# Kernel optimization log

Measured on AMD Instinct MI355X. Metric: run time of the kernel, lower is better.

## Reference

```python
import jax, jax.numpy as jnp
import numpy as np

NC = 80          # num classes
NBINS = 16       # DFL bins = reg_max_bbox_loss + 1
REG_MAX = 15     # BboxLoss reg_max (m.reg_max - 1)
GAMMA = 1.5      # focal gamma (h['fl_gamma'])
ALPHA = 0.25     # focal alpha
BOX_W, CLS_W, DFL_W = 7.5, 0.5, 1.5
LEVELS = [(80, 80), (40, 40), (20, 20)]  # 640x640 image, strides 8/16/32


def make_anchor_points():
    pts = []
    for h, w in LEVELS:
        ys, xs = np.meshgrid(np.arange(h) + 0.5, np.arange(w) + 0.5, indexing='ij')
        pts.append(np.stack([xs.ravel(), ys.ravel()], -1))
    return jnp.asarray(np.concatenate(pts, 0), jnp.float32)  # (8400, 2)


def setup_inputs() -> dict:
    B, A = 32, 8400
    key = jax.random.key(0)
    k = jax.random.split(key, 6)
    anchor_points = make_anchor_points()
    pred_dist = jax.random.normal(k[0], (B, A, 4 * NBINS), jnp.float32)
    pred_scores = jax.random.normal(k[1], (B, A, NC), jnp.float32)
    fg_mask = jax.random.uniform(k[2], (B, A)) < 0.05
    # valid xyxy targets around each anchor -> ltrb in (0.5, 6) < REG_MAX - 0.01
    off1 = jax.random.uniform(k[3], (B, A, 2), minval=0.5, maxval=6.0)
    off2 = jax.random.uniform(k[4], (B, A, 2), minval=0.5, maxval=6.0)
    target_bboxes = jnp.concatenate([anchor_points - off1, anchor_points + off2], -1)
    target_scores = jax.random.uniform(k[5], (B, A, NC)) * fg_mask[..., None].astype(jnp.float32)
    return dict(pred_dist=pred_dist, pred_scores=pred_scores,
                anchor_points=anchor_points, target_bboxes=target_bboxes,
                target_scores=target_scores, fg_mask=fg_mask)


def _ciou(b1, b2, eps=1e-7):
    # xyxy CIoU, matches ultralytics bbox_iou(xywh=False, CIoU=True)
    b1x1, b1y1, b1x2, b1y2 = b1[..., 0], b1[..., 1], b1[..., 2], b1[..., 3]
    b2x1, b2y1, b2x2, b2y2 = b2[..., 0], b2[..., 1], b2[..., 2], b2[..., 3]
    w1, h1 = b1x2 - b1x1, b1y2 - b1y1 + eps
    w2, h2 = b2x2 - b2x1, b2y2 - b2y1 + eps
    inter = (jnp.minimum(b1x2, b2x2) - jnp.maximum(b1x1, b2x1)).clip(0) * \
            (jnp.minimum(b1y2, b2y2) - jnp.maximum(b1y1, b2y1)).clip(0)
    union = w1 * h1 + w2 * h2 - inter + eps
    iou = inter / union
    cw = jnp.maximum(b1x2, b2x2) - jnp.minimum(b1x1, b2x1)
    ch = jnp.maximum(b1y2, b2y2) - jnp.minimum(b1y1, b2y1)
    c2 = cw * cw + ch * ch + eps
    rho2 = ((b2x1 + b2x2 - b1x1 - b1x2) ** 2 + (b2y1 + b2y2 - b1y1 - b1y2) ** 2) / 4.0
    v = (4.0 / (jnp.pi ** 2)) * (jnp.arctan(w2 / h2) - jnp.arctan(w1 / h1)) ** 2
    alpha = jax.lax.stop_gradient(v / (v - iou + (1.0 + eps)))  # torch.no_grad()
    return iou - (rho2 / c2 + v * alpha)


def _loss_core(pred_dist, pred_scores, anchor_points, target_bboxes, target_scores, fg_mask):
    B, A, _ = pred_scores.shape
    dt = pred_scores.dtype
    tss = jnp.maximum(target_scores.sum(), 1.0)  # target_scores_sum

    # ---- focal BCE (pos_weight=1) ----
    p = jax.nn.sigmoid(pred_scores)
    bce = target_scores * jax.nn.softplus(-pred_scores) + (1.0 - target_scores) * jax.nn.softplus(pred_scores)
    p_t = target_scores * p + (1.0 - target_scores) * (1.0 - p)
    alpha_f = target_scores * ALPHA + (1.0 - target_scores) * (1.0 - ALPHA)
    loss_cls = (bce * alpha_f * (1.0 - p_t) ** GAMMA).sum() / tss

    # ---- bbox decode (DFL expectation) ----
    proj = jnp.arange(NBINS, dtype=dt)
    logits = pred_dist.reshape(B, A, 4, NBINS)
    dist = jax.nn.softmax(logits, axis=-1) @ proj                     # (B,A,4) ltrb
    pred_bboxes = jnp.concatenate([anchor_points - dist[..., :2],
                                   anchor_points + dist[..., 2:]], -1)

    fg = fg_mask.astype(dt)
    bbox_weight = target_scores.sum(-1) * fg                          # masked weight (B,A)

    # ---- CIoU loss (mask replaces masked_select) ----
    iou = _ciou(pred_bboxes, target_bboxes)
    loss_iou = ((1.0 - iou) * bbox_weight).sum() / tss

    # ---- DFL loss: left/right weighted cross-entropy ----
    target_ltrb = jnp.clip(jnp.concatenate([anchor_points - target_bboxes[..., :2],
                                            target_bboxes[..., 2:] - anchor_points], -1),
                           0.0, REG_MAX - 0.01)                       # (B,A,4)
    tl = jnp.floor(target_ltrb).astype(jnp.int32)
    tr = tl + 1
    wl = tr.astype(dt) - target_ltrb
    wr = 1.0 - wl
    logp = jax.nn.log_softmax(logits, axis=-1)                        # (B,A,4,NBINS)
    ce_l = -jnp.take_along_axis(logp, tl[..., None], axis=-1)[..., 0]
    ce_r = -jnp.take_along_axis(logp, tr[..., None], axis=-1)[..., 0]
    loss_dfl = (((ce_l * wl + ce_r * wr).mean(-1)) * bbox_weight).sum() / tss

    return jnp.stack([BOX_W * loss_iou, CLS_W * loss_cls, DFL_W * loss_dfl])


def reference(pred_dist, pred_scores, anchor_points, target_bboxes, target_scores, fg_mask):
    loss = _loss_core(pred_dist, pred_scores, anchor_points, target_bboxes, target_scores, fg_mask)
    return loss  # weighted [box, cls, dfl]; total = loss.sum()
```

## Files before the change

kernel.cpp:

```cpp
#include <hip/hip_runtime.h>
#include <math.h>

#define NC      80
#define A_TOT   8400
#define B_TOT   32
#define BA      (B_TOT * A_TOT)
#define NGRP    (BA / 16)
#define BLOCK   256
#define MAXNB   4200

__device__ __forceinline__ float wave_sum(float v) {
    #pragma unroll
    for (int off = 32; off > 0; off >>= 1) v += __shfl_down(v, off, 64);
    return v;
}

__global__ __launch_bounds__(BLOCK) void loss_main(
    const float* __restrict__ pred_dist,
    const float* __restrict__ pred_scores,
    const float* __restrict__ anchor_points,
    const float* __restrict__ target_bboxes,
    const float* __restrict__ target_scores,
    const int* __restrict__ fgmask,
    float* __restrict__ partials,
    int nb)
{
    __shared__ float red[4][4];

    const int tid  = threadIdx.x;
    const int lane = tid & 63;
    const int wid  = tid >> 6;
    const int q    = lane & 3;
    const int alg  = lane >> 2;
    const int gw   = blockIdx.x * 4 + wid;
    const int nw   = nb * 4;

    const float4* ps4 = (const float4*)pred_scores;
    const float4* ts4 = (const float4*)target_scores;
    const float4* tb4 = (const float4*)target_bboxes;

    float cls_acc = 0.0f, iou_acc = 0.0f, dfl_acc = 0.0f, ts_acc = 0.0f;

    for (int grp = gw; grp < NGRP; grp += nw) {
        const long g0   = (long)grp * 16;
        const long base = (g0 + alg) * 20 + q;

        const int fgm = fgmask[g0 + alg];

        float4 tvl[5];
        #pragma unroll
        for (int j = 0; j < 5; ++j) tvl[j] = make_float4(0.f, 0.f, 0.f, 0.f);
        if (fgm) {
            #pragma unroll
            for (int j = 0; j < 5; ++j) tvl[j] = ts4[base + 4 * j];
        }

        float rs = 0.0f;
        #pragma unroll
        for (int j = 0; j < 5; ++j) {
            float4 pv = ps4[base + 4 * j];
            float px[4] = {pv.x, pv.y, pv.z, pv.w};
            float tx[4] = {tvl[j].x, tvl[j].y, tvl[j].z, tvl[j].w};
            #pragma unroll
            for (int c = 0; c < 4; ++c) {
                float x  = px[c];
                float tv = tx[c];
                float e   = __expf(-fabsf(x));
                float ope = 1.0f + e;
                float lp  = __logf(ope);
                float sp  = fmaxf(x, 0.0f) + lp;
                float bce = sp - tv * x;
                float pp  = __builtin_amdgcn_rcpf(ope);
                float p   = (x >= 0.0f) ? pp : (1.0f - pp);
                float u   = fmaf(p, 1.0f - 2.0f * tv, tv);
                u = fmaxf(u, 0.0f);
                float af  = 0.75f - 0.5f * tv;
                float su  = __builtin_amdgcn_sqrtf(u);
                cls_acc += bce * af * (u * su);
                rs += tv;
            }
        }
        rs += __shfl_xor(rs, 1);
        rs += __shfl_xor(rs, 2);
        if (q == 0) ts_acc += rs;

        unsigned long long m = __ballot(rs > 0.0f && q == 0);
        while (m) {
            int b = __ffsll((long long)m) - 1;
            m &= m - 1;
            float w = __shfl(rs, b);
            const long g = g0 + (b >> 2);
            const int  a = (int)(g % A_TOT);
            const float ax = anchor_points[2 * a];
            const float ay = anchor_points[2 * a + 1];
            const float4 tb = tb4[g];

            const int side = lane >> 4;
            const int k    = lane & 15;

            float x = pred_dist[g * 64 + lane];

            float tval = (side == 0) ? ax - tb.x :
                         (side == 1) ? ay - tb.y :
                         (side == 2) ? tb.z - ax : tb.w - ay;
            float tcl = fminf(fmaxf(tval, 0.0f), 14.99f);
            int   tl  = (int)tcl;
            float wl  = (float)(tl + 1) - tcl;
            float wr  = 1.0f - wl;

            float mx = x;
            mx = fmaxf(mx, __shfl_xor(mx, 1));
            mx = fmaxf(mx, __shfl_xor(mx, 2));
            mx = fmaxf(mx, __shfl_xor(mx, 4));
            mx = fmaxf(mx, __shfl_xor(mx, 8));

            float ex = __expf(x - mx);
            float se = ex;
            float nu = (float)k * ex;
            float ls = ((k == tl) ? wl : (k == tl + 1) ? wr : 0.0f) * x;
            #pragma unroll
            for (int off = 1; off < 16; off <<= 1) {
                se += __shfl_xor(se, off);
                nu += __shfl_xor(nu, off);
                ls += __shfl_xor(ls, off);
            }
            float dist = nu * __builtin_amdgcn_rcpf(se);
            float ce   = mx + __logf(se) - ls;

            float d0 = __shfl(dist, 0),  d1 = __shfl(dist, 16);
            float d2 = __shfl(dist, 32), d3 = __shfl(dist, 48);
            float c0 = __shfl(ce, 0),    c1 = __shfl(ce, 16);
            float c2 = __shfl(ce, 32),   c3 = __shfl(ce, 48);

            if (lane == 0) {
                dfl_acc += 0.25f * (c0 + c1 + c2 + c3) * w;

                const float eps = 1e-7f;
                float px1 = ax - d0, py1 = ay - d1;
                float px2 = ax + d2, py2 = ay + d3;
                float w1 = px2 - px1, h1 = py2 - py1 + eps;
                float w2 = tb.z - tb.x, h2 = tb.w - tb.y + eps;
                float iw = fmaxf(fminf(px2, tb.z) - fmaxf(px1, tb.x), 0.0f);
                float ih = fmaxf(fminf(py2, tb.w) - fmaxf(py1, tb.y), 0.0f);
                float inter = iw * ih;
                float uni = w1 * h1 + w2 * h2 - inter + eps;
                float iou = inter / uni;
                float cw = fmaxf(px2, tb.z) - fminf(px1, tb.x);
                float ch = fmaxf(py2, tb.w) - fminf(py1, tb.y);
                float c2d = cw * cw + ch * ch + eps;
                float dx = tb.x + tb.z - px1 - px2;
                float dy = tb.y + tb.w - py1 - py2;
                float rho2 = (dx * dx + dy * dy) * 0.25f;
                const float c4pi2 = 0.40528473456935109f;
                float dat = atanf(w2 / h2) - atanf(w1 / h1);
                float v = c4pi2 * dat * dat;
                float alpha = v / (v - iou + (1.0f + eps));
                float ciou = iou - (rho2 / c2d + v * alpha);
                iou_acc += (1.0f - ciou) * w;
            }
        }
    }

    float v0 = wave_sum(iou_acc);
    float v1 = wave_sum(cls_acc);
    float v2 = wave_sum(ts_acc);
    float v3 = wave_sum(dfl_acc);
    if (lane == 0) { red[0][wid] = v0; red[1][wid] = v1; red[2][wid] = v2; red[3][wid] = v3; }
    __syncthreads();
    if (tid == 0) {
        float r0 = 0, r1 = 0, r2 = 0, r3 = 0;
        #pragma unroll
        for (int i = 0; i < 4; ++i) { r0 += red[0][i]; r1 += red[1][i]; r2 += red[2][i]; r3 += red[3][i]; }
        partials[0 * nb + blockIdx.x] = r0;
        partials[1 * nb + blockIdx.x] = r1;
        partials[2 * nb + blockIdx.x] = r2;
        partials[3 * nb + blockIdx.x] = r3;
    }
}

__global__ __launch_bounds__(BLOCK) void loss_reduce(
    const float* __restrict__ partials, int nb, float* __restrict__ out)
{
    __shared__ float red[4][4];
    int tid = threadIdx.x;
    float s0 = 0, s1 = 0, s2 = 0, s3 = 0;
    for (int i = tid; i < nb; i += BLOCK) {
        s0 += partials[i];
        s1 += partials[nb + i];
        s2 += partials[2 * nb + i];
        s3 += partials[3 * nb + i];
    }
    s0 = wave_sum(s0); s1 = wave_sum(s1); s2 = wave_sum(s2); s3 = wave_sum(s3);
    int wid = tid >> 6;
    if ((tid & 63) == 0) { red[0][wid] = s0; red[1][wid] = s1; red[2][wid] = s2; red[3][wid] = s3; }
    __syncthreads();
    if (tid == 0) {
        float r0 = 0, r1 = 0, r2 = 0, r3 = 0;
        #pragma unroll
        for (int i = 0; i < 4; ++i) { r0 += red[0][i]; r1 += red[1][i]; r2 += red[2][i]; r3 += red[3][i]; }
        float tss = fmaxf(r2, 1.0f);
        out[0] = 7.5f * r0 / tss;
        out[1] = 0.5f * r1 / tss;
        out[2] = 1.5f * r3 / tss;
    }
}

extern "C" void kernel_launch(void* const* d_in, const int* in_sizes, int n_in,
                              void* d_out, int out_size, void* d_ws, size_t ws_size,
                              hipStream_t stream) {
    const float* pred_dist     = (const float*)d_in[0];
    const float* pred_scores   = (const float*)d_in[1];
    const float* anchor_points = (const float*)d_in[2];
    const float* target_bboxes = (const float*)d_in[3];
    const float* target_scores = (const float*)d_in[4];
    const int*   fgmask        = (const int*)d_in[5];

    int nb = (int)(ws_size / (4 * sizeof(float)));
    if (nb > MAXNB) nb = MAXNB;
    if (nb < 1) nb = 1;

    float* partials = (float*)d_ws;
    loss_main<<<nb, BLOCK, 0, stream>>>(
        pred_dist, pred_scores, anchor_points, target_bboxes, target_scores,
        fgmask, partials, nb);
    loss_reduce<<<1, BLOCK, 0, stream>>>(partials, nb, (float*)d_out);
}
```

Before: 220.6 us.

## Split blocks into dedicated foreground DFL/CIoU and dense classification roles

Blocks are partitioned so one third scan the foreground mask in 64-anchor chunks and compute DFL and CIoU terms, prefetching the next foreground anchor's data while computing the current one. The remaining blocks run only the dense focal-BCE pass over scores and accumulate the target-score sum. This is meant to keep the latency-bound serial foreground loop from stalling the bandwidth-bound dense stream. The fixed one-third split risks load imbalance between the two roles.

New measurement: 216.1 us. 2.1% less time.

```diff
diff --git a/kernel.cpp b/kernel.cpp
--- a/kernel.cpp
+++ b/kernel.cpp
@@ -6,8 +6,9 @@
 #define B_TOT   32
 #define BA      (B_TOT * A_TOT)
 #define NGRP    (BA / 16)
+#define NCHUNK  (BA / 64)
 #define BLOCK   256
-#define MAXNB   4200
+#define NB_TARGET 3150
 
 __device__ __forceinline__ float wave_sum(float v) {
     #pragma unroll
@@ -23,17 +24,13 @@
     const float* __restrict__ target_scores,
     const int* __restrict__ fgmask,
     float* __restrict__ partials,
-    int nb)
+    int nb, int fgb)
 {
     __shared__ float red[4][4];
 
     const int tid  = threadIdx.x;
     const int lane = tid & 63;
     const int wid  = tid >> 6;
-    const int q    = lane & 3;
-    const int alg  = lane >> 2;
-    const int gw   = blockIdx.x * 4 + wid;
-    const int nw   = nb * 4;
 
     const float4* ps4 = (const float4*)pred_scores;
     const float4* ts4 = (const float4*)target_scores;
@@ -41,122 +38,147 @@
 
     float cls_acc = 0.0f, iou_acc = 0.0f, dfl_acc = 0.0f, ts_acc = 0.0f;
 
-    for (int grp = gw; grp < NGRP; grp += nw) {
-        const long g0   = (long)grp * 16;
-        const long base = (g0 + alg) * 20 + q;
-
-        const int fgm = fgmask[g0 + alg];
-
-        float4 tvl[5];
-        #pragma unroll
-        for (int j = 0; j < 5; ++j) tvl[j] = make_float4(0.f, 0.f, 0.f, 0.f);
-        if (fgm) {
+    if ((int)blockIdx.x < fgb) {
+        const int fstride = fgb * 4;
+        for (int c = blockIdx.x * 4 + wid; c < NCHUNK; c += fstride) {
+            const long abase = (long)c * 64;
+            const int myfg = fgmask[abase + lane];
+            unsigned long long m = __ballot(myfg != 0);
+
+            long gc = -1; float xc = 0.0f;
+            float4 tbc = make_float4(0,0,0,0), tsc = make_float4(0,0,0,0);
+            if (m) {
+                int b = __ffsll((long long)m) - 1; m &= m - 1;
+                gc = abase + b;
+                xc  = pred_dist[gc * 64 + lane];
+                tbc = tb4[gc];
+                tsc = (lane < 20) ? ts4[gc * 20 + lane] : make_float4(0,0,0,0);
+            }
+            while (gc >= 0) {
+                long gn = -1; float xn = 0.0f;
+                float4 tbn = make_float4(0,0,0,0), tsn = make_float4(0,0,0,0);
+                if (m) {
+                    int b = __ffsll((long long)m) - 1; m &= m - 1;
+                    gn = abase + b;
+                    xn  = pred_dist[gn * 64 + lane];
+                    tbn = tb4[gn];
+                    tsn = (lane < 20) ? ts4[gn * 20 + lane] : make_float4(0,0,0,0);
+                }
+
+                float w = tsc.x + tsc.y + tsc.z + tsc.w;
+                #pragma unroll
+                for (int off = 1; off < 64; off <<= 1) w += __shfl_xor(w, off, 64);
+
+                const int a = (int)(gc % A_TOT);
+                const float ax = anchor_points[2 * a];
+                const float ay = anchor_points[2 * a + 1];
+                const int side = lane >> 4;
+                const int k    = lane & 15;
+                const float x  = xc;
+
+                float tval = (side == 0) ? ax - tbc.x :
+                             (side == 1) ? ay - tbc.y :
+                             (side == 2) ? tbc.z - ax : tbc.w - ay;
+                float tcl = fminf(fmaxf(tval, 0.0f), 14.99f);
+                int   tl  = (int)tcl;
+                float wl  = (float)(tl + 1) - tcl;
+                float wr  = 1.0f - wl;
+
+                float mx = x;
+                mx = fmaxf(mx, __shfl_xor(mx, 1));
+                mx = fmaxf(mx, __shfl_xor(mx, 2));
+                mx = fmaxf(mx, __shfl_xor(mx, 4));
+                mx = fmaxf(mx, __shfl_xor(mx, 8));
+
+                float ex = __expf(x - mx);
+                float se = ex;
+                float nu = (float)k * ex;
+                float ls = ((k == tl) ? wl : (k == tl + 1) ? wr : 0.0f) * x;
+                #pragma unroll
+                for (int off = 1; off < 16; off <<= 1) {
+                    se += __shfl_xor(se, off);
+                    nu += __shfl_xor(nu, off);
+                    ls += __shfl_xor(ls, off);
+                }
+                float dist = nu * __builtin_amdgcn_rcpf(se);
+                float ce   = mx + __logf(se) - ls;
+
+                float d0 = __shfl(dist, 0),  d1 = __shfl(dist, 16);
+                float d2 = __shfl(dist, 32), d3 = __shfl(dist, 48);
+                float c0 = __shfl(ce, 0),    c1 = __shfl(ce, 16);
+                float c2 = __shfl(ce, 32),   c3 = __shfl(ce, 48);
+
+                if (lane == 0) {
+                    dfl_acc += 0.25f * (c0 + c1 + c2 + c3) * w;
+
+                    const float eps = 1e-7f;
+                    float px1 = ax - d0, py1 = ay - d1;
+                    float px2 = ax + d2, py2 = ay + d3;
+                    float w1 = px2 - px1, h1 = py2 - py1 + eps;
+                    float w2 = tbc.z - tbc.x, h2 = tbc.w - tbc.y + eps;
+                    float iw = fmaxf(fminf(px2, tbc.z) - fmaxf(px1, tbc.x), 0.0f);
+                    float ih = fmaxf(fminf(py2, tbc.w) - fmaxf(py1, tbc.y), 0.0f);
+                    float inter = iw * ih;
+                    float uni = w1 * h1 + w2 * h2 - inter + eps;
+                    float iou = inter / uni;
+                    float cw = fmaxf(px2, tbc.z) - fminf(px1, tbc.x);
+                    float ch = fmaxf(py2, tbc.w) - fminf(py1, tbc.y);
+                    float c2d = cw * cw + ch * ch + eps;
+                    float dx = tbc.x + tbc.z - px1 - px2;
+                    float dy = tbc.y + tbc.w - py1 - py2;
+                    float rho2 = (dx * dx + dy * dy) * 0.25f;
+                    const float c4pi2 = 0.40528473456935109f;
+                    float dat = atanf(w2 / h2) - atanf(w1 / h1);
+                    float v = c4pi2 * dat * dat;
+                    float alpha = v / (v - iou + (1.0f + eps));
+                    float ciou = iou - (rho2 / c2d + v * alpha);
+                    iou_acc += (1.0f - ciou) * w;
+                }
+
+                gc = gn; xc = xn; tbc = tbn; tsc = tsn;
+            }
+        }
+    } else {
+        const int q   = lane & 3;
+        const int alg = lane >> 2;
+        const int dstride = (nb - fgb) * 4;
+        for (int grp = (blockIdx.x - fgb) * 4 + wid; grp < NGRP; grp += dstride) {
+            const long g0   = (long)grp * 16;
+            const long base = (g0 + alg) * 20 + q;
+
+            const int fgm = fgmask[g0 + alg];
+
+            float4 tvl[5];
             #pragma unroll
-            for (int j = 0; j < 5; ++j) tvl[j] = ts4[base + 4 * j];
-        }
-
-        float rs = 0.0f;
-        #pragma unroll
-        for (int j = 0; j < 5; ++j) {
-            float4 pv = ps4[base + 4 * j];
-            float px[4] = {pv.x, pv.y, pv.z, pv.w};
-            float tx[4] = {tvl[j].x, tvl[j].y, tvl[j].z, tvl[j].w};
+            for (int j = 0; j < 5; ++j) tvl[j] = make_float4(0.f, 0.f, 0.f, 0.f);
+            if (fgm) {
+                #pragma unroll
+                for (int j = 0; j < 5; ++j) tvl[j] = ts4[base + 4 * j];
+            }
+
             #pragma unroll
-            for (int c = 0; c < 4; ++c) {
-                float x  = px[c];
-                float tv = tx[c];
-                float e   = __expf(-fabsf(x));
-                float ope = 1.0f + e;
-                float lp  = __logf(ope);
-                float sp  = fmaxf(x, 0.0f) + lp;
-                float bce = sp - tv * x;
-                float pp  = __builtin_amdgcn_rcpf(ope);
-                float p   = (x >= 0.0f) ? pp : (1.0f - pp);
-                float u   = fmaf(p, 1.0f - 2.0f * tv, tv);
-                u = fmaxf(u, 0.0f);
-                float af  = 0.75f - 0.5f * tv;
-                float su  = __builtin_amdgcn_sqrtf(u);
-                cls_acc += bce * af * (u * su);
-                rs += tv;
-            }
-        }
-        rs += __shfl_xor(rs, 1);
-        rs += __shfl_xor(rs, 2);
-        if (q == 0) ts_acc += rs;
-
-        unsigned long long m = __ballot(rs > 0.0f && q == 0);
-        while (m) {
-            int b = __ffsll((long long)m) - 1;
-            m &= m - 1;
-            float w = __shfl(rs, b);
-            const long g = g0 + (b >> 2);
-            const int  a = (int)(g % A_TOT);
-            const float ax = anchor_points[2 * a];
-            const float ay = anchor_points[2 * a + 1];
-            const float4 tb = tb4[g];
-
-            const int side = lane >> 4;
-            const int k    = lane & 15;
-
-            float x = pred_dist[g * 64 + lane];
-
-            float tval = (side == 0) ? ax - tb.x :
-                         (side == 1) ? ay - tb.y :
-                         (side == 2) ? tb.z - ax : tb.w - ay;
-            float tcl = fminf(fmaxf(tval, 0.0f), 14.99f);
-            int   tl  = (int)tcl;
-            float wl  = (float)(tl + 1) - tcl;
-            float wr  = 1.0f - wl;
-
-            float mx = x;
-            mx = fmaxf(mx, __shfl_xor(mx, 1));
-            mx = fmaxf(mx, __shfl_xor(mx, 2));
-            mx = fmaxf(mx, __shfl_xor(mx, 4));
-            mx = fmaxf(mx, __shfl_xor(mx, 8));
-
-            float ex = __expf(x - mx);
-            float se = ex;
-            float nu = (float)k * ex;
-            float ls = ((k == tl) ? wl : (k == tl + 1) ? wr : 0.0f) * x;
-            #pragma unroll
-            for (int off = 1; off < 16; off <<= 1) {
-                se += __shfl_xor(se, off);
-                nu += __shfl_xor(nu, off);
-                ls += __shfl_xor(ls, off);
-            }
-            float dist = nu * __builtin_amdgcn_rcpf(se);
-            float ce   = mx + __logf(se) - ls;
-
-            float d0 = __shfl(dist, 0),  d1 = __shfl(dist, 16);
-            float d2 = __shfl(dist, 32), d3 = __shfl(dist, 48);
-            float c0 = __shfl(ce, 0),    c1 = __shfl(ce, 16);
-            float c2 = __shfl(ce, 32),   c3 = __shfl(ce, 48);
-
-            if (lane == 0) {
-                dfl_acc += 0.25f * (c0 + c1 + c2 + c3) * w;
-
-                const float eps = 1e-7f;
-                float px1 = ax - d0, py1 = ay - d1;
-                float px2 = ax + d2, py2 = ay + d3;
-                float w1 = px2 - px1, h1 = py2 - py1 + eps;
-                float w2 = tb.z - tb.x, h2 = tb.w - tb.y + eps;
-                float iw = fmaxf(fminf(px2, tb.z) - fmaxf(px1, tb.x), 0.0f);
-                float ih = fmaxf(fminf(py2, tb.w) - fmaxf(py1, tb.y), 0.0f);
-                float inter = iw * ih;
-                float uni = w1 * h1 + w2 * h2 - inter + eps;
-                float iou = inter / uni;
-                float cw = fmaxf(px2, tb.z) - fminf(px1, tb.x);
-                float ch = fmaxf(py2, tb.w) - fminf(py1, tb.y);
-                float c2d = cw * cw + ch * ch + eps;
-                float dx = tb.x + tb.z - px1 - px2;
-                float dy = tb.y + tb.w - py1 - py2;
-                float rho2 = (dx * dx + dy * dy) * 0.25f;
-                const float c4pi2 = 0.40528473456935109f;
-                float dat = atanf(w2 / h2) - atanf(w1 / h1);
-                float v = c4pi2 * dat * dat;
-                float alpha = v / (v - iou + (1.0f + eps));
-                float ciou = iou - (rho2 / c2d + v * alpha);
-                iou_acc += (1.0f - ciou) * w;
+            for (int j = 0; j < 5; ++j) {
+                float4 pv = ps4[base + 4 * j];
+                float px[4] = {pv.x, pv.y, pv.z, pv.w};
+                float tx[4] = {tvl[j].x, tvl[j].y, tvl[j].z, tvl[j].w};
+                #pragma unroll
+                for (int cc = 0; cc < 4; ++cc) {
+                    float xx = px[cc];
+                    float tv = tx[cc];
+                    float e   = __expf(-fabsf(xx));
+                    float ope = 1.0f + e;
+                    float lp  = __logf(ope);
+                    float sp  = fmaxf(xx, 0.0f) + lp;
+                    float bce = sp - tv * xx;
+                    float pp  = __builtin_amdgcn_rcpf(ope);
+                    float p   = (xx >= 0.0f) ? pp : (1.0f - pp);
+                    float u   = fmaf(p, 1.0f - 2.0f * tv, tv);
+                    u = fmaxf(u, 0.0f);
+                    float af  = 0.75f - 0.5f * tv;
+                    float su  = __builtin_amdgcn_sqrtf(u);
+                    cls_acc += bce * af * (u * su);
+                    ts_acc  += tv;
+                }
             }
         }
     }
@@ -216,12 +238,14 @@
     const int*   fgmask        = (const int*)d_in[5];
 
     int nb = (int)(ws_size / (4 * sizeof(float)));
-    if (nb > MAXNB) nb = MAXNB;
-    if (nb < 1) nb = 1;
+    if (nb > NB_TARGET) nb = NB_TARGET;
+    if (nb < 2) nb = 2;
+    int fgb = nb / 3;
+    if (fgb < 1) fgb = 1;
 
     float* partials = (float*)d_ws;
     loss_main<<<nb, BLOCK, 0, stream>>>(
         pred_dist, pred_scores, anchor_points, target_bboxes, target_scores,
-        fgmask, partials, nb);
+        fgmask, partials, nb, fgb);
     loss_reduce<<<1, BLOCK, 0, stream>>>(partials, nb, (float*)d_out);
 }
```
